# Optimization experiments

Hardware: AMD Instinct MI355X
Metric: run time of the kernel (lower is better)

Reference implementation:

```python
import jax, jax.numpy as jnp
import numpy as np

N = 50000      # nodes
E = 600000     # edges (avg degree 12)
D_IN = 16      # node_input_size
D = 128        # hidden_size
H = 4          # num_heads
DH = D // H
L = 4          # message_passing_num
D_FF = 512     # 4*hidden FFN expansion
D_OUT = 3      # output_size


def setup_inputs() -> dict:
    key = jax.random.key(0)
    ks = iter(jax.random.split(key, 32))
    def w(shape, fan_in):
        return jax.random.normal(next(ks), shape, jnp.float32) / np.float32(np.sqrt(fan_in))
    return {
        "features": jax.random.normal(next(ks), (N, D_IN), jnp.float32),
        "senders": jax.random.randint(next(ks), (E,), 0, N),
        "receivers": jax.random.randint(next(ks), (E,), 0, N),
        "enc_w1": w((D_IN, D), D_IN), "enc_b1": jnp.zeros((D,), jnp.float32),
        "enc_w2": w((D, D), D),       "enc_b2": jnp.zeros((D,), jnp.float32),
        "wq": w((L, D, D), D), "wk": w((L, D, D), D),
        "wv": w((L, D, D), D), "wo": w((L, D, D), D),
        "ln1_s": jnp.ones((L, D), jnp.float32), "ln1_b": jnp.zeros((L, D), jnp.float32),
        "ffn_w1": w((L, D, D_FF), D), "ffn_b1": jnp.zeros((L, D_FF), jnp.float32),
        "ffn_w2": w((L, D_FF, D), D_FF), "ffn_b2": jnp.zeros((L, D), jnp.float32),
        "ln2_s": jnp.ones((L, D), jnp.float32), "ln2_b": jnp.zeros((L, D), jnp.float32),
        "dec_w1": w((D, D_OUT), D), "dec_b1": jnp.zeros((D_OUT,), jnp.float32),
        "dec_w2": w((D_OUT, D_OUT), D_OUT), "dec_b2": jnp.zeros((D_OUT,), jnp.float32),
    }


def _ln(x, s, b):
    mu = x.mean(-1, keepdims=True)
    var = ((x - mu) ** 2).mean(-1, keepdims=True)
    return (x - mu) * jax.lax.rsqrt(var + 1e-5) * s + b


def _graph_mha(x, senders, receivers, wq, wk, wv, wo):
    # Adjacency-masked attention done sparsely over the edge list
    # (equivalent to softmax over the BCOO adjacency pattern).
    n = x.shape[0]
    q = (x @ wq).reshape(n, H, DH)
    k = (x @ wk).reshape(n, H, DH)
    v = (x @ wv).reshape(n, H, DH)
    scores = (q[receivers] * k[senders]).sum(-1) / np.float32(np.sqrt(DH))  # [E,H]
    m = jax.ops.segment_max(scores, receivers, num_segments=n)             # [N,H]
    m = jnp.where(jnp.isfinite(m), m, 0.0)
    a = jnp.exp(scores - m[receivers])                                      # [E,H]
    denom = jax.ops.segment_sum(a, receivers, num_segments=n)              # [N,H]
    msg = jax.ops.segment_sum(a[:, :, None] * v[senders], receivers, num_segments=n)  # [N,H,DH]
    out = (msg / (denom[:, :, None] + 1e-9)).reshape(n, D)
    return out @ wo


def reference(features, senders, receivers,
              enc_w1, enc_b1, enc_w2, enc_b2,
              wq, wk, wv, wo, ln1_s, ln1_b,
              ffn_w1, ffn_b1, ffn_w2, ffn_b2, ln2_s, ln2_b,
              dec_w1, dec_b1, dec_w2, dec_b2):
    # encode
    x = jnp.maximum(features @ enc_w1 + enc_b1, 0.0) @ enc_w2 + enc_b2     # [N,D]
    # process: L pre-LN sparse-attention transformer blocks
    for l in range(L):
        h = _ln(x, ln1_s[l], ln1_b[l])
        x = x + _graph_mha(h, senders, receivers, wq[l], wk[l], wv[l], wo[l])
        h = _ln(x, ln2_s[l], ln2_b[l])
        x = x + jnp.maximum(h @ ffn_w1[l] + ffn_b1[l], 0.0) @ ffn_w2[l] + ffn_b2[l]
    # decode
    return jnp.maximum(x @ dec_w1 + dec_b1, 0.0) @ dec_w2 + dec_b2         # [N,D_OUT]
```

## Files before the change

kernel.cpp:

```cpp
#include <hip/hip_runtime.h>
#include <hip/hip_bf16.h>
#include <math.h>

#define D     128
#define NHEAD 4
#define DH    32
#define DFF   512
#define DIN   16
#define MAXDEG 64
#define TN    16

typedef __attribute__((ext_vector_type(8))) short bf16x8;
typedef __attribute__((ext_vector_type(4))) float f32x4;
typedef __hip_bfloat16 bf16;

#define QSCALE_L2E 0.2550348838f

#define AP 132
#define BM 64

__global__ void k_fill(const int* __restrict__ recv, const int* __restrict__ senders,
                       int* __restrict__ deg, int* __restrict__ eid, int E) {
    int e = blockIdx.x * blockDim.x + threadIdx.x;
    if (e >= E) return;
    int r = recv[e];
    int pos = atomicAdd(&deg[r], 1);
    if (pos < MAXDEG) eid[r * MAXDEG + pos] = senders[e];
}

__global__ void k_wt(const float* __restrict__ wq, const float* __restrict__ wk,
                     const float* __restrict__ wv, const float* __restrict__ wo,
                     const float* __restrict__ w1, const float* __restrict__ w2,
                     const float* __restrict__ encw2,
                     bf16* __restrict__ wqkvT, bf16* __restrict__ woT,
                     bf16* __restrict__ w1T, bf16* __restrict__ w2T,
                     bf16* __restrict__ encw2T, int* __restrict__ deg, int N) {
    int r = blockIdx.y;
    if (r == 25) {
        int i = blockIdx.x * blockDim.x + threadIdx.x;
        if (i < N) deg[i] = 0;
        return;
    }
    const float* src; bf16* dst; int K, Nout;
    if (r < 12) {
        int l = r / 3, sel = r % 3;
        src = (sel == 0 ? wq : sel == 1 ? wk : wv) + (size_t)l * D * D;
        dst = wqkvT + (size_t)l * 3 * D * D + (size_t)sel * D * D;
        K = D; Nout = D;
    } else if (r < 16) {
        int l = r - 12;
        src = wo + (size_t)l * D * D; dst = woT + (size_t)l * D * D; K = D; Nout = D;
    } else if (r < 20) {
        int l = r - 16;
        src = w1 + (size_t)l * D * DFF; dst = w1T + (size_t)l * D * DFF; K = D; Nout = DFF;
    } else if (r < 24) {
        int l = r - 20;
        src = w2 + (size_t)l * DFF * D; dst = w2T + (size_t)l * DFF * D; K = DFF; Nout = D;
    } else {
        src = encw2; dst = encw2T; K = D; Nout = D;
    }
    int total = K * Nout;
    int i = blockIdx.x * blockDim.x + threadIdx.x;
    if (i >= total) return;
    int k = i / Nout, j = i % Nout;
    dst[(size_t)j * K + k] = __float2bfloat16(src[i]);
}

__device__ __forceinline__ void load_afrag(const bf16* A, int arow, int quad,
                                           int N, bf16x8* afr) {
    const bf16* ab = A + (size_t)arow * D + quad * 8;
#pragma unroll
    for (int i = 0; i < 4; i++) {
        uint4 v = make_uint4(0u, 0u, 0u, 0u);
        if (arow < N) v = *(const uint4*)(ab + i * 32);
        afr[i] = *(bf16x8*)&v;
    }
}

template<int OP>
__global__ __launch_bounds__(256) void k_gemm(
        const bf16* __restrict__ A, const bf16* __restrict__ Bt,
        const float* __restrict__ bias,
        const float* __restrict__ lns, const float* __restrict__ lnb,
        float* x, bf16* outB, int N) {
    __shared__ alignas(16) bf16 Wsm[128][AP];
    int m0 = blockIdx.x * BM;
    int t = threadIdx.x;
    int wave = t >> 6, lane = t & 63;
    int quad = lane >> 4, l16 = lane & 15;
    int wm = wave * 16;

    bf16x8 afr[4];
    load_afrag(A, m0 + wm + l16, quad, N, afr);
#pragma unroll
    for (int it = 0; it < 8; it++) {
        int ci = it * 256 + t;
        int rr = ci >> 4, cc = (ci & 15) * 8;
        *(uint4*)&Wsm[rr][cc] = *(const uint4*)(Bt + (size_t)rr * D + cc);
    }
    __syncthreads();

    f32x4 acc[8];
#pragma unroll
    for (int j = 0; j < 8; j++) acc[j] = (f32x4){0.f, 0.f, 0.f, 0.f};
#pragma unroll
    for (int i = 0; i < 4; i++) {
#pragma unroll
        for (int j = 0; j < 8; j++) {
            bf16x8 bfr = *(const bf16x8*)&Wsm[j * 16 + l16][i * 32 + quad * 8];
            acc[j] = __builtin_amdgcn_mfma_f32_16x16x32_bf16(afr[i], bfr, acc[j], 0, 0, 0);
        }
    }

    int rowb = m0 + wm + quad * 4;
    float bv[8];
    if (OP == 5) {
#pragma unroll
        for (int j = 0; j < 8; j++) bv[j] = bias[j * 16 + l16];
    }
#pragma unroll
    for (int j = 0; j < 8; j++) {
        int col = j * 16 + l16;
#pragma unroll
        for (int r = 0; r < 4; r++) {
            int gr = rowb + r;
            if (gr >= N) continue;
            float val = acc[j][r];
            if (OP == 5) val += bv[j];
            if (OP == 2) val += x[(size_t)gr * D + col];
            acc[j][r] = val;
        }
    }
    float lsv[8], lbv[8];
#pragma unroll
    for (int j = 0; j < 8; j++) {
        lsv[j] = lns[j * 16 + l16];
        lbv[j] = lnb[j * 16 + l16];
    }
#pragma unroll
    for (int r = 0; r < 4; r++) {
        float s1 = 0.f, s2 = 0.f;
#pragma unroll
        for (int j = 0; j < 8; j++) {
            float v = acc[j][r];
            s1 += v; s2 += v * v;
        }
        s1 += __shfl_xor(s1, 1, 64);  s2 += __shfl_xor(s2, 1, 64);
        s1 += __shfl_xor(s1, 2, 64);  s2 += __shfl_xor(s2, 2, 64);
        s1 += __shfl_xor(s1, 4, 64);  s2 += __shfl_xor(s2, 4, 64);
        s1 += __shfl_xor(s1, 8, 64);  s2 += __shfl_xor(s2, 8, 64);
        float mu = s1 * (1.f / 128.f);
        float var = s2 * (1.f / 128.f) - mu * mu;
        float rinv = rsqrtf(fmaxf(var, 0.f) + 1e-5f);
        int gr = rowb + r;
        if (gr >= N) continue;
#pragma unroll
        for (int j = 0; j < 8; j++) {
            int col = j * 16 + l16;
            float v = acc[j][r];
            x[(size_t)gr * D + col] = v;
            outB[(size_t)gr * D + col] =
                __float2bfloat16((v - mu) * rinv * lsv[j] + lbv[j]);
        }
    }
}

__global__ __launch_bounds__(256) void k_qkv(
        const bf16* __restrict__ hb, const bf16* __restrict__ wqkvT,
        bf16* __restrict__ qb, bf16* __restrict__ kvb, int N) {
    __shared__ alignas(16) bf16 Wsm[128][AP];
    int m0 = blockIdx.x * BM;
    int t = threadIdx.x;
    int wave = t >> 6, lane = t & 63;
    int quad = lane >> 4, l16 = lane & 15;
    int wm = wave * 16;

    bf16x8 afr[4];
    load_afrag(hb, m0 + wm + l16, quad, N, afr);

    for (int y = 0; y < 3; y++) {
        const bf16* W = wqkvT + (size_t)y * D * D;
#pragma unroll
        for (int it = 0; it < 8; it++) {
            int ci = it * 256 + t;
            int rr = ci >> 4, cc = (ci & 15) * 8;
            *(uint4*)&Wsm[rr][cc] = *(const uint4*)(W + (size_t)rr * D + cc);
        }
        __syncthreads();

        f32x4 acc[8];
#pragma unroll
        for (int j = 0; j < 8; j++) acc[j] = (f32x4){0.f, 0.f, 0.f, 0.f};
#pragma unroll
        for (int i = 0; i < 4; i++) {
#pragma unroll
            for (int j = 0; j < 8; j++) {
                bf16x8 bfr = *(const bf16x8*)&Wsm[j * 16 + l16][i * 32 + quad * 8];
                acc[j] = __builtin_amdgcn_mfma_f32_16x16x32_bf16(afr[i], bfr, acc[j], 0, 0, 0);
            }
        }
        int rowb = m0 + wm + quad * 4;
#pragma unroll
        for (int j = 0; j < 8; j++) {
            int col = j * 16 + l16;
#pragma unroll
            for (int r = 0; r < 4; r++) {
                int gr = rowb + r;
                if (gr >= N) continue;
                float val = acc[j][r];
                if (y == 0) qb[(size_t)gr * D + col] = __float2bfloat16(val * QSCALE_L2E);
                else kvb[((size_t)gr * D + col) * 2 + (y - 1)] = __float2bfloat16(val);
            }
        }
        if (y < 2) __syncthreads();
    }
}

template<int MODE>
__global__ __launch_bounds__(256) void k_ffn(
        const bf16* __restrict__ hb, const bf16* __restrict__ w1T,
        const float* __restrict__ b1,
        const bf16* __restrict__ w2T, const float* __restrict__ b2,
        const float* __restrict__ lns, const float* __restrict__ lnb,
        const float* __restrict__ dw1, const float* __restrict__ db1,
        const float* __restrict__ dw2, const float* __restrict__ db2,
        float* x, bf16* outB, float* out, int N) {
    __shared__ alignas(16) bf16 Wsm[128][AP];
    __shared__ alignas(16) bf16 Hsm[64][AP];
    int m0 = blockIdx.x * 64;
    int t = threadIdx.x;
    int wave = t >> 6, lane = t & 63;
    int quad = lane >> 4, l16 = lane & 15;
    int wm = wave * 16;

    bf16x8 afr[4];
    load_afrag(hb, m0 + wm + l16, quad, N, afr);
#pragma unroll
    for (int it = 0; it < 8; it++) {
        int ci = it * 256 + t;
        int rr = ci >> 4, cc = (ci & 15) * 8;
        *(uint4*)&Wsm[rr][cc] = *(const uint4*)(w1T + (size_t)rr * D + cc);
    }
    __syncthreads();

    f32x4 acc2[8];
#pragma unroll
    for (int j = 0; j < 8; j++) acc2[j] = (f32x4){0.f, 0.f, 0.f, 0.f};

    for (int c = 0; c < 4; c++) {
        f32x4 accP[8];
#pragma unroll
        for (int j = 0; j < 8; j++) accP[j] = (f32x4){0.f, 0.f, 0.f, 0.f};
#pragma unroll
        for (int i = 0; i < 4; i++) {
#pragma unroll
            for (int j = 0; j < 8; j++) {
                bf16x8 bfr = *(const bf16x8*)&Wsm[j * 16 + l16][i * 32 + quad * 8];
                accP[j] = __builtin_amdgcn_mfma_f32_16x16x32_bf16(afr[i], bfr, accP[j], 0, 0, 0);
            }
        }
        __syncthreads();
#pragma unroll
        for (int it = 0; it < 8; it++) {
            int ci = it * 256 + t;
            int rr = ci >> 4, cc = (ci & 15) * 8;
            *(uint4*)&Wsm[rr][cc] = *(const uint4*)(w2T + (size_t)rr * DFF + c * 128 + cc);
        }
        {
            float bv[8];
#pragma unroll
            for (int j = 0; j < 8; j++) bv[j] = b1[c * 128 + j * 16 + l16];
            int rw = wm + quad * 4;
#pragma unroll
            for (int j = 0; j < 8; j++) {
                int col = j * 16 + l16;
#pragma unroll
                for (int r = 0; r < 4; r++)
                    Hsm[rw + r][col] = __float2bfloat16(fmaxf(accP[j][r] + bv[j], 0.f));
            }
        }
        __syncthreads();
#pragma unroll
        for (int ks = 0; ks < 4; ks++) {
            bf16x8 af2 = *(const bf16x8*)&Hsm[wm + l16][ks * 32 + quad * 8];
#pragma unroll
            for (int j = 0; j < 8; j++) {
                bf16x8 bfr = *(const bf16x8*)&Wsm[j * 16 + l16][ks * 32 + quad * 8];
                acc2[j] = __builtin_amdgcn_mfma_f32_16x16x32_bf16(af2, bfr, acc2[j], 0, 0, 0);
            }
        }
        if (c < 3) {
            __syncthreads();
#pragma unroll
            for (int it = 0; it < 8; it++) {
                int ci = it * 256 + t;
                int rr = ci >> 4, cc = (ci & 15) * 8;
                *(uint4*)&Wsm[rr][cc] =
                    *(const uint4*)(w1T + (size_t)((c + 1) * 128 + rr) * D + cc);
            }
            __syncthreads();
        }
    }

    int rowb = m0 + wm + quad * 4;
    float bv[8];
#pragma unroll
    for (int j = 0; j < 8; j++) bv[j] = b2[j * 16 + l16];
#pragma unroll
    for (int j = 0; j < 8; j++) {
        int col = j * 16 + l16;
#pragma unroll
        for (int r = 0; r < 4; r++) {
            int gr = rowb + r;
            if (gr >= N) continue;
            acc2[j][r] += bv[j] + x[(size_t)gr * D + col];
        }
    }
    if (MODE == 1) {
        float dw[8][3];
#pragma unroll
        for (int j = 0; j < 8; j++) {
            int col = j * 16 + l16;
#pragma unroll
            for (int cc3 = 0; cc3 < 3; cc3++) dw[j][cc3] = dw1[col * 3 + cc3];
        }
#pragma unroll
        for (int r = 0; r < 4; r++) {
            float s0 = 0.f, s1 = 0.f, s2 = 0.f;
#pragma unroll
            for (int j = 0; j < 8; j++) {
                float v = acc2[j][r];
                s0 += v * dw[j][0]; s1 += v * dw[j][1]; s2 += v * dw[j][2];
            }
            s0 += __shfl_xor(s0, 1, 64); s1 += __shfl_xor(s1, 1, 64); s2 += __shfl_xor(s2, 1, 64);
            s0 += __shfl_xor(s0, 2, 64); s1 += __shfl_xor(s1, 2, 64); s2 += __shfl_xor(s2, 2, 64);
            s0 += __shfl_xor(s0, 4, 64); s1 += __shfl_xor(s1, 4, 64); s2 += __shfl_xor(s2, 4, 64);
            s0 += __shfl_xor(s0, 8, 64); s1 += __shfl_xor(s1, 8, 64); s2 += __shfl_xor(s2, 8, 64);
            int gr = rowb + r;
            if (l16 == 0 && gr < N) {
                float t0 = fmaxf(s0 + db1[0], 0.f);
                float t1 = fmaxf(s1 + db1[1], 0.f);
                float t2 = fmaxf(s2 + db1[2], 0.f);
#pragma unroll
                for (int o = 0; o < 3; o++)
                    out[(size_t)gr * 3 + o] =
                        t0 * dw2[0 * 3 + o] + t1 * dw2[1 * 3 + o] + t2 * dw2[2 * 3 + o] + db2[o];
            }
        }
        return;
    }
    float lsv[8], lbv[8];
#pragma unroll
    for (int j = 0; j < 8; j++) {
        lsv[j] = lns[j * 16 + l16];
        lbv[j] = lnb[j * 16 + l16];
    }
#pragma unroll
    for (int r = 0; r < 4; r++) {
        float s1 = 0.f, s2 = 0.f;
#pragma unroll
        for (int j = 0; j < 8; j++) {
            float v = acc2[j][r];
            s1 += v; s2 += v * v;
        }
        s1 += __shfl_xor(s1, 1, 64);  s2 += __shfl_xor(s2, 1, 64);
        s1 += __shfl_xor(s1, 2, 64);  s2 += __shfl_xor(s2, 2, 64);
        s1 += __shfl_xor(s1, 4, 64);  s2 += __shfl_xor(s2, 4, 64);
        s1 += __shfl_xor(s1, 8, 64);  s2 += __shfl_xor(s2, 8, 64);
        float mu = s1 * (1.f / 128.f);
        float var = s2 * (1.f / 128.f) - mu * mu;
        float rinv = rsqrtf(fmaxf(var, 0.f) + 1e-5f);
        int gr = rowb + r;
        if (gr >= N) continue;
#pragma unroll
        for (int j = 0; j < 8; j++) {
            int col = j * 16 + l16;
            float v = acc2[j][r];
            x[(size_t)gr * D + col] = v;
            outB[(size_t)gr * D + col] = __float2bfloat16((v - mu) * rinv * lsv[j] + lbv[j]);
        }
    }
}

__global__ void k_enc1(const float* __restrict__ feat,
                       const float* __restrict__ w1, const float* __restrict__ b1,
                       bf16* __restrict__ hb, int N) {
    __shared__ float fsh[TN][DIN];
    int n0 = blockIdx.x * TN;
    int j = threadIdx.x;
    int nvalid = min(TN, N - n0);
    for (int idx = j; idx < TN * DIN; idx += 128) {
        int n = idx / DIN, i = idx % DIN;
        fsh[n][i] = (n < nvalid) ? feat[(n0 + n) * DIN + i] : 0.f;
    }
    __syncthreads();
    float bb = b1[j];
#pragma unroll
    for (int n = 0; n < TN; n++) {
        float a = bb;
#pragma unroll
        for (int i = 0; i < DIN; i++) a += fsh[n][i] * w1[i * D + j];
        if (n < nvalid) hb[(size_t)(n0 + n) * D + j] = __float2bfloat16(fmaxf(a, 0.f));
    }
}

__device__ __forceinline__ void attn_edge(uint4 w, bool v, float4 qv,
                                          float& l, float& a0, float& a1,
                                          float& a2, float& a3) {
    float k0 = __uint_as_float(w.x << 16), v0 = __uint_as_float(w.x & 0xFFFF0000u);
    float k1 = __uint_as_float(w.y << 16), v1 = __uint_as_float(w.y & 0xFFFF0000u);
    float k2 = __uint_as_float(w.z << 16), v2 = __uint_as_float(w.z & 0xFFFF0000u);
    float k3 = __uint_as_float(w.w << 16), v3 = __uint_as_float(w.w & 0xFFFF0000u);
    float p = qv.x * k0 + qv.y * k1 + qv.z * k2 + qv.w * k3;
    p += __shfl_xor(p, 1, 64);
    p += __shfl_xor(p, 2, 64);
    p += __shfl_xor(p, 4, 64);
    float e = v ? exp2f(p) : 0.f;
    l += e;
    a0 += e * v0; a1 += e * v1; a2 += e * v2; a3 += e * v3;
}

__global__ __launch_bounds__(256) void k_attn(
        const bf16* __restrict__ qb, const uint* __restrict__ kvb,
        const int* __restrict__ deg, const int* __restrict__ eid,
        bf16* __restrict__ out, int N) {
    int wave = threadIdx.x >> 6, lane = threadIdx.x & 63;
    int r = blockIdx.x * 4 + wave;
    if (r >= N) return;
    int g = lane & 7;
    int h = (lane >> 3) & 3;
    int slot = lane >> 5;
    int d0 = h * 32 + g * 4;
    uint2 qw = *(const uint2*)(qb + (size_t)r * D + d0);
    float4 qv;
    qv.x = __uint_as_float(qw.x << 16);
    qv.y = __uint_as_float(qw.x & 0xFFFF0000u);
    qv.z = __uint_as_float(qw.y << 16);
    qv.w = __uint_as_float(qw.y & 0xFFFF0000u);
    int cnt = min(deg[r], MAXDEG);
    const int* row = eid + (size_t)r * MAXDEG;
    float l = 0.f, a0 = 0.f, a1 = 0.f, a2 = 0.f, a3 = 0.f;
    for (int base = 0; base < cnt; base += 8) {
        int ei[4];
        bool vv[4];
        int ss[4];
#pragma unroll
        for (int u = 0; u < 4; u++) {
            ei[u] = base + u * 2 + slot;
            vv[u] = ei[u] < cnt;
            ss[u] = vv[u] ? row[ei[u]] : 0;
        }
        uint4 w0 = *(const uint4*)(kvb + (size_t)ss[0] * D + d0);
        uint4 w1 = *(const uint4*)(kvb + (size_t)ss[1] * D + d0);
        uint4 w2 = *(const uint4*)(kvb + (size_t)ss[2] * D + d0);
        uint4 w3 = *(const uint4*)(kvb + (size_t)ss[3] * D + d0);
        attn_edge(w0, vv[0], qv, l, a0, a1, a2, a3);
        attn_edge(w1, vv[1], qv, l, a0, a1, a2, a3);
        attn_edge(w2, vv[2], qv, l, a0, a1, a2, a3);
        attn_edge(w3, vv[3], qv, l, a0, a1, a2, a3);
    }
    l  += __shfl_xor(l, 32, 64);
    a0 += __shfl_xor(a0, 32, 64);
    a1 += __shfl_xor(a1, 32, 64);
    a2 += __shfl_xor(a2, 32, 64);
    a3 += __shfl_xor(a3, 32, 64);
    if (lane < 32) {
        float inv = 1.f / (l + 1e-9f);
        bf16 o[4];
        o[0] = __float2bfloat16(a0 * inv);
        o[1] = __float2bfloat16(a1 * inv);
        o[2] = __float2bfloat16(a2 * inv);
        o[3] = __float2bfloat16(a3 * inv);
        *(uint2*)(out + (size_t)r * D + d0) = *(uint2*)o;
    }
}

extern "C" void kernel_launch(void* const* d_in, const int* in_sizes, int n_in,
                              void* d_out, int out_size, void* d_ws, size_t ws_size,
                              hipStream_t stream) {
    const float* feat    = (const float*)d_in[0];
    const int*   senders = (const int*)d_in[1];
    const int*   recv    = (const int*)d_in[2];
    const float* enc_w1  = (const float*)d_in[3];
    const float* enc_b1  = (const float*)d_in[4];
    const float* enc_w2  = (const float*)d_in[5];
    const float* enc_b2  = (const float*)d_in[6];
    const float* wq      = (const float*)d_in[7];
    const float* wk      = (const float*)d_in[8];
    const float* wv      = (const float*)d_in[9];
    const float* wo      = (const float*)d_in[10];
    const float* ln1_s   = (const float*)d_in[11];
    const float* ln1_b   = (const float*)d_in[12];
    const float* ffn_w1  = (const float*)d_in[13];
    const float* ffn_b1  = (const float*)d_in[14];
    const float* ffn_w2  = (const float*)d_in[15];
    const float* ffn_b2  = (const float*)d_in[16];
    const float* ln2_s   = (const float*)d_in[17];
    const float* ln2_b   = (const float*)d_in[18];
    const float* dec_w1  = (const float*)d_in[19];
    const float* dec_b1  = (const float*)d_in[20];
    const float* dec_w2  = (const float*)d_in[21];
    const float* dec_b2  = (const float*)d_in[22];

    int N = in_sizes[0] / DIN;
    int E = in_sizes[1];

    char* p = (char*)d_ws;
    float* x   = (float*)p;  p += (size_t)N * D * 4;
    bf16*  qb  = (bf16*)p;   p += (size_t)N * D * 2;
    bf16*  kvb = (bf16*)p;   p += (size_t)N * D * 2 * 2;
    bf16*  hb  = (bf16*)p;   p += (size_t)N * D * 2;
    int* deg   = (int*)p;    p += (size_t)N * 4;
    int* eid   = (int*)p;    p += (size_t)N * MAXDEG * 4;
    bf16* wqkvT  = (bf16*)p; p += (size_t)4 * 3 * D * D * 2;
    bf16* woT    = (bf16*)p; p += (size_t)4 * D * D * 2;
    bf16* w1T    = (bf16*)p; p += (size_t)4 * D * DFF * 2;
    bf16* w2T    = (bf16*)p; p += (size_t)4 * DFF * D * 2;
    bf16* encw2T = (bf16*)p; p += (size_t)D * D * 2;

    int gm = (N + BM - 1) / BM;

    k_wt<<<dim3(256, 26), 256, 0, stream>>>(wq, wk, wv, wo, ffn_w1, ffn_w2, enc_w2,
                                            wqkvT, woT, w1T, w2T, encw2T, deg, N);
    k_fill<<<(E + 255) / 256, 256, 0, stream>>>(recv, senders, deg, eid, E);
    k_enc1<<<(N + TN - 1) / TN, 128, 0, stream>>>(feat, enc_w1, enc_b1, hb, N);
    k_gemm<5><<<gm, 256, 0, stream>>>(hb, encw2T, enc_b2, ln1_s, ln1_b, x, hb, N);

    for (int l = 0; l < 4; l++) {
        k_qkv<<<gm, 256, 0, stream>>>(hb, wqkvT + (size_t)l * 3 * D * D, qb, kvb, N);
        k_attn<<<(N + 3) / 4, 256, 0, stream>>>(qb, (const uint*)kvb, deg, eid, hb, N);
        k_gemm<2><<<gm, 256, 0, stream>>>(hb, woT + (size_t)l * D * D,
                                          nullptr, ln2_s + l * D, ln2_b + l * D,
                                          x, hb, N);
        if (l < 3)
            k_ffn<0><<<gm, 256, 0, stream>>>(hb, w1T + (size_t)l * D * DFF,
                                             ffn_b1 + l * DFF,
                                             w2T + (size_t)l * DFF * D, ffn_b2 + l * D,
                                             ln1_s + (l + 1) * D, ln1_b + (l + 1) * D,
                                             nullptr, nullptr, nullptr, nullptr,
                                             x, hb, nullptr, N);
        else
            k_ffn<1><<<gm, 256, 0, stream>>>(hb, w1T + (size_t)l * D * DFF,
                                             ffn_b1 + l * DFF,
                                             w2T + (size_t)l * DFF * D, ffn_b2 + l * D,
                                             nullptr, nullptr,
                                             dec_w1, dec_b1, dec_w2, dec_b2,
                                             x, nullptr, (float*)d_out, N);
    }
}
```

Measured before the change: 728.5 us.

## Stage GEMM weights via async global-to-LDS loads with swizzle and multi-buffering

Replaces register-staged weight copies into padded LDS with direct global_load_lds transfers into XOR-swizzled unpadded tiles. The QKV kernel double-buffers the three weight matrices and the FFN kernel runs a 16-step, triple-buffered half-tile pipeline so weight loads overlap MFMA work. It also prefetches residual x values early, packs K/V stores into one 32-bit write, and raises wave priority around MFMA sections. The intent is to hide weight-load latency and cut LDS bank conflicts. In exchange it relies on hand-placed vmcnt waits and barriers, which are fragile if the load counts change.

```diff
diff --git a/kernel.cpp b/kernel.cpp
--- a/kernel.cpp
+++ b/kernel.cpp
@@ -16,8 +16,23 @@
 
 #define QSCALE_L2E 0.2550348838f
 
-#define AP 132
 #define BM 64
+
+#define WAITV(N) asm volatile("s_waitcnt vmcnt(" #N ")" ::: "memory")
+#define WAITLGKM asm volatile("s_waitcnt lgkmcnt(0)" ::: "memory")
+#define FENCE()  asm volatile("" ::: "memory")
+#define BAR() do { FENCE(); __builtin_amdgcn_s_barrier(); FENCE(); } while (0)
+
+__device__ __forceinline__ void gll16(const bf16* g, bf16* l) {
+    __builtin_amdgcn_global_load_lds((__attribute__((address_space(1))) void*)g,
+                                     (__attribute__((address_space(3))) void*)l,
+                                     16, 0, 0);
+}
+
+__device__ __forceinline__ ushort bfbits(float f) {
+    __hip_bfloat16 b = __float2bfloat16(f);
+    return *(ushort*)&b;
+}
 
 __global__ void k_fill(const int* __restrict__ recv, const int* __restrict__ senders,
                        int* __restrict__ deg, int* __restrict__ eid, int E) {
@@ -77,13 +92,48 @@
     }
 }
 
+__device__ __forceinline__ void stage_full(bf16* lb, const bf16* src,
+                                           int wave, int lane) {
+#pragma unroll
+    for (int k = 0; k < 8; k++) {
+        int gidx = (wave * 8 + k) * 64 + lane;
+        int r = gidx >> 4, gL = gidx & 15;
+        gll16(src + (size_t)r * 128 + ((gL ^ (r & 15)) * 8),
+              lb + (size_t)(wave * 8 + k) * 512);
+    }
+}
+
+__device__ __forceinline__ void stage_half(bf16* lb, const bf16* src, int rs,
+                                           int wave, int lane) {
+#pragma unroll
+    for (int k = 0; k < 4; k++) {
+        int gidx = (wave * 4 + k) * 64 + lane;
+        int r = gidx >> 3, gL = gidx & 7;
+        gll16(src + (size_t)r * rs + ((gL ^ (r & 7)) * 8),
+              lb + (size_t)(wave * 4 + k) * 512);
+    }
+}
+
+__device__ __forceinline__ void mfma_tile(const bf16* Wb, const bf16x8* afr,
+                                          f32x4* acc, int l16, int quad) {
+#pragma unroll
+    for (int i = 0; i < 4; i++)
+#pragma unroll
+        for (int j = 0; j < 8; j++) {
+            const bf16* wp = Wb + (size_t)(j * 16 + l16) * 128
+                              + (size_t)((((i * 4 + quad)) ^ l16) * 8);
+            acc[j] = __builtin_amdgcn_mfma_f32_16x16x32_bf16(afr[i], *(const bf16x8*)wp,
+                                                             acc[j], 0, 0, 0);
+        }
+}
+
 template<int OP>
 __global__ __launch_bounds__(256) void k_gemm(
         const bf16* __restrict__ A, const bf16* __restrict__ Bt,
         const float* __restrict__ bias,
         const float* __restrict__ lns, const float* __restrict__ lnb,
         float* x, bf16* outB, int N) {
-    __shared__ alignas(16) bf16 Wsm[128][AP];
+    __shared__ alignas(16) bf16 Wsm[128 * 128];
     int m0 = blockIdx.x * BM;
     int t = threadIdx.x;
     int wave = t >> 6, lane = t & 63;
@@ -92,27 +142,27 @@
 
     bf16x8 afr[4];
     load_afrag(A, m0 + wm + l16, quad, N, afr);
-#pragma unroll
-    for (int it = 0; it < 8; it++) {
-        int ci = it * 256 + t;
-        int rr = ci >> 4, cc = (ci & 15) * 8;
-        *(uint4*)&Wsm[rr][cc] = *(const uint4*)(Bt + (size_t)rr * D + cc);
-    }
-    __syncthreads();
+    FENCE();
+    stage_full(Wsm, Bt, wave, lane);
+    WAITV(0); BAR();
+
+    int rowb = m0 + wm + quad * 4;
+    float xv[8][4];
+    if (OP == 2) {
+#pragma unroll
+        for (int j = 0; j < 8; j++)
+#pragma unroll
+            for (int r = 0; r < 4; r++) {
+                int gr = rowb + r;
+                xv[j][r] = (gr < N) ? x[(size_t)gr * D + j * 16 + l16] : 0.f;
+            }
+    }
 
     f32x4 acc[8];
 #pragma unroll
     for (int j = 0; j < 8; j++) acc[j] = (f32x4){0.f, 0.f, 0.f, 0.f};
-#pragma unroll
-    for (int i = 0; i < 4; i++) {
-#pragma unroll
-        for (int j = 0; j < 8; j++) {
-            bf16x8 bfr = *(const bf16x8*)&Wsm[j * 16 + l16][i * 32 + quad * 8];
-            acc[j] = __builtin_amdgcn_mfma_f32_16x16x32_bf16(afr[i], bfr, acc[j], 0, 0, 0);
-        }
-    }
-
-    int rowb = m0 + wm + quad * 4;
+    mfma_tile(Wsm, afr, acc, l16, quad);
+
     float bv[8];
     if (OP == 5) {
 #pragma unroll
@@ -120,14 +170,13 @@
     }
 #pragma unroll
     for (int j = 0; j < 8; j++) {
-        int col = j * 16 + l16;
 #pragma unroll
         for (int r = 0; r < 4; r++) {
             int gr = rowb + r;
             if (gr >= N) continue;
             float val = acc[j][r];
             if (OP == 5) val += bv[j];
-            if (OP == 2) val += x[(size_t)gr * D + col];
+            if (OP == 2) val += xv[j][r];
             acc[j][r] = val;
         }
     }
@@ -168,7 +217,7 @@
 __global__ __launch_bounds__(256) void k_qkv(
         const bf16* __restrict__ hb, const bf16* __restrict__ wqkvT,
         bf16* __restrict__ qb, bf16* __restrict__ kvb, int N) {
-    __shared__ alignas(16) bf16 Wsm[128][AP];
+    __shared__ alignas(16) bf16 Wbuf[2][128 * 128];
     int m0 = blockIdx.x * BM;
     int t = threadIdx.x;
     int wave = t >> 6, lane = t & 63;
@@ -177,43 +226,59 @@
 
     bf16x8 afr[4];
     load_afrag(hb, m0 + wm + l16, quad, N, afr);
-
-    for (int y = 0; y < 3; y++) {
-        const bf16* W = wqkvT + (size_t)y * D * D;
-#pragma unroll
-        for (int it = 0; it < 8; it++) {
-            int ci = it * 256 + t;
-            int rr = ci >> 4, cc = (ci & 15) * 8;
-            *(uint4*)&Wsm[rr][cc] = *(const uint4*)(W + (size_t)rr * D + cc);
-        }
-        __syncthreads();
-
-        f32x4 acc[8];
-#pragma unroll
-        for (int j = 0; j < 8; j++) acc[j] = (f32x4){0.f, 0.f, 0.f, 0.f};
-#pragma unroll
-        for (int i = 0; i < 4; i++) {
-#pragma unroll
-            for (int j = 0; j < 8; j++) {
-                bf16x8 bfr = *(const bf16x8*)&Wsm[j * 16 + l16][i * 32 + quad * 8];
-                acc[j] = __builtin_amdgcn_mfma_f32_16x16x32_bf16(afr[i], bfr, acc[j], 0, 0, 0);
-            }
-        }
-        int rowb = m0 + wm + quad * 4;
-#pragma unroll
-        for (int j = 0; j < 8; j++) {
-            int col = j * 16 + l16;
-#pragma unroll
-            for (int r = 0; r < 4; r++) {
-                int gr = rowb + r;
-                if (gr >= N) continue;
-                float val = acc[j][r];
-                if (y == 0) qb[(size_t)gr * D + col] = __float2bfloat16(val * QSCALE_L2E);
-                else kvb[((size_t)gr * D + col) * 2 + (y - 1)] = __float2bfloat16(val);
-            }
-        }
-        if (y < 2) __syncthreads();
-    }
+    FENCE();
+    stage_full(Wbuf[0], wqkvT, wave, lane);
+    FENCE();
+    stage_full(Wbuf[1], wqkvT + (size_t)D * D, wave, lane);
+    FENCE();
+
+    f32x4 aq[8], ak[8], av[8];
+#pragma unroll
+    for (int j = 0; j < 8; j++) aq[j] = (f32x4){0.f, 0.f, 0.f, 0.f};
+
+    WAITV(8); BAR();
+    __builtin_amdgcn_s_setprio(1);
+    mfma_tile(Wbuf[0], afr, aq, l16, quad);
+    __builtin_amdgcn_s_setprio(0);
+    BAR();
+    stage_full(Wbuf[0], wqkvT + (size_t)2 * D * D, wave, lane);
+    FENCE();
+    WAITV(8); BAR();
+#pragma unroll
+    for (int j = 0; j < 8; j++) ak[j] = (f32x4){0.f, 0.f, 0.f, 0.f};
+    __builtin_amdgcn_s_setprio(1);
+    mfma_tile(Wbuf[1], afr, ak, l16, quad);
+    __builtin_amdgcn_s_setprio(0);
+    WAITV(0); BAR();
+#pragma unroll
+    for (int j = 0; j < 8; j++) av[j] = (f32x4){0.f, 0.f, 0.f, 0.f};
+    __builtin_amdgcn_s_setprio(1);
+    mfma_tile(Wbuf[0], afr, av, l16, quad);
+    __builtin_amdgcn_s_setprio(0);
+
+    int rowb = m0 + wm + quad * 4;
+#pragma unroll
+    for (int j = 0; j < 8; j++) {
+        int col = j * 16 + l16;
+#pragma unroll
+        for (int r = 0; r < 4; r++) {
+            int gr = rowb + r;
+            if (gr >= N) continue;
+            qb[(size_t)gr * D + col] = __float2bfloat16(aq[j][r] * QSCALE_L2E);
+            uint kv = (uint)bfbits(ak[j][r]) | ((uint)bfbits(av[j][r]) << 16);
+            *(uint*)&kvb[((size_t)gr * D + col) * 2] = kv;
+        }
+    }
+}
+
+__device__ __forceinline__ void stage_ffn_tile(int ts, const bf16* w1T,
+                                               const bf16* w2T, bf16* Wb3,
+                                               int wave, int lane) {
+    int c = ts >> 2, ph = ts & 3;
+    const bf16* src; int rs;
+    if (ph < 2) { src = w1T + (size_t)(c * 128) * 128 + ph * 64; rs = 128; }
+    else        { src = w2T + c * 128 + (ph - 2) * 64;           rs = DFF; }
+    stage_half(Wb3 + (size_t)(ts % 3) * (64 * 128), src, rs, wave, lane);
 }
 
 template<int MODE>
@@ -225,95 +290,115 @@
         const float* __restrict__ dw1, const float* __restrict__ db1,
         const float* __restrict__ dw2, const float* __restrict__ db2,
         float* x, bf16* outB, float* out, int N) {
-    __shared__ alignas(16) bf16 Wsm[128][AP];
-    __shared__ alignas(16) bf16 Hsm[64][AP];
+    __shared__ alignas(16) bf16 Wb3[3][64 * 128];
+    __shared__ alignas(16) bf16 Hsm[64 * 128];
     int m0 = blockIdx.x * 64;
     int t = threadIdx.x;
     int wave = t >> 6, lane = t & 63;
     int quad = lane >> 4, l16 = lane & 15;
     int wm = wave * 16;
+    int rowb = m0 + wm + quad * 4;
+
+    float b1pre[4][8];
+#pragma unroll
+    for (int c2 = 0; c2 < 4; c2++)
+#pragma unroll
+        for (int j = 0; j < 8; j++) b1pre[c2][j] = b1[c2 * 128 + j * 16 + l16];
 
     bf16x8 afr[4];
     load_afrag(hb, m0 + wm + l16, quad, N, afr);
-#pragma unroll
-    for (int it = 0; it < 8; it++) {
-        int ci = it * 256 + t;
-        int rr = ci >> 4, cc = (ci & 15) * 8;
-        *(uint4*)&Wsm[rr][cc] = *(const uint4*)(w1T + (size_t)rr * D + cc);
-    }
-    __syncthreads();
-
-    f32x4 acc2[8];
+    FENCE();
+    stage_ffn_tile(0, w1T, w2T, &Wb3[0][0], wave, lane);
+    FENCE();
+    stage_ffn_tile(1, w1T, w2T, &Wb3[0][0], wave, lane);
+    FENCE();
+
+    f32x4 acc2[8], accP[8];
 #pragma unroll
     for (int j = 0; j < 8; j++) acc2[j] = (f32x4){0.f, 0.f, 0.f, 0.f};
-
-    for (int c = 0; c < 4; c++) {
-        f32x4 accP[8];
-#pragma unroll
-        for (int j = 0; j < 8; j++) accP[j] = (f32x4){0.f, 0.f, 0.f, 0.f};
-#pragma unroll
-        for (int i = 0; i < 4; i++) {
-#pragma unroll
-            for (int j = 0; j < 8; j++) {
-                bf16x8 bfr = *(const bf16x8*)&Wsm[j * 16 + l16][i * 32 + quad * 8];
-                accP[j] = __builtin_amdgcn_mfma_f32_16x16x32_bf16(afr[i], bfr, accP[j], 0, 0, 0);
+    float xv[8][4];
+
+#pragma unroll
+    for (int s = 0; s < 16; s++) {
+        if (s < 15) { WAITV(4); } else { WAITV(0); }
+        BAR();
+        if (s + 2 < 16) {
+            stage_ffn_tile(s + 2, w1T, w2T, &Wb3[0][0], wave, lane);
+            FENCE();
+        }
+        const bf16* Wb = &Wb3[0][0] + (size_t)(s % 3) * (64 * 128);
+        int c = s >> 2, ph = s & 3;
+        if (s == 15) {
+#pragma unroll
+            for (int j = 0; j < 8; j++)
+#pragma unroll
+                for (int r = 0; r < 4; r++) {
+                    int gr = rowb + r;
+                    xv[j][r] = (gr < N) ? x[(size_t)gr * D + j * 16 + l16] : 0.f;
+                }
+        }
+        if (ph < 2) {
+            if (ph == 0) {
+#pragma unroll
+                for (int j = 0; j < 8; j++) accP[j] = (f32x4){0.f, 0.f, 0.f, 0.f};
             }
-        }
-        __syncthreads();
-#pragma unroll
-        for (int it = 0; it < 8; it++) {
-            int ci = it * 256 + t;
-            int rr = ci >> 4, cc = (ci & 15) * 8;
-            *(uint4*)&Wsm[rr][cc] = *(const uint4*)(w2T + (size_t)rr * DFF + c * 128 + cc);
-        }
-        {
-            float bv[8];
-#pragma unroll
-            for (int j = 0; j < 8; j++) bv[j] = b1[c * 128 + j * 16 + l16];
-            int rw = wm + quad * 4;
-#pragma unroll
-            for (int j = 0; j < 8; j++) {
-                int col = j * 16 + l16;
-#pragma unroll
-                for (int r = 0; r < 4; r++)
-                    Hsm[rw + r][col] = __float2bfloat16(fmaxf(accP[j][r] + bv[j], 0.f));
+            __builtin_amdgcn_s_setprio(1);
+#pragma unroll
+            for (int i2 = 0; i2 < 2; i2++) {
+#pragma unroll
+                for (int j = 0; j < 8; j++) {
+                    const bf16* wp = Wb + (size_t)(j * 16 + l16) * 64
+                                      + (size_t)(((i2 * 4 + quad) ^ (l16 & 7)) * 8);
+                    accP[j] = __builtin_amdgcn_mfma_f32_16x16x32_bf16(
+                        afr[ph * 2 + i2], *(const bf16x8*)wp, accP[j], 0, 0, 0);
+                }
             }
-        }
-        __syncthreads();
-#pragma unroll
-        for (int ks = 0; ks < 4; ks++) {
-            bf16x8 af2 = *(const bf16x8*)&Hsm[wm + l16][ks * 32 + quad * 8];
-#pragma unroll
-            for (int j = 0; j < 8; j++) {
-                bf16x8 bfr = *(const bf16x8*)&Wsm[j * 16 + l16][ks * 32 + quad * 8];
-                acc2[j] = __builtin_amdgcn_mfma_f32_16x16x32_bf16(af2, bfr, acc2[j], 0, 0, 0);
+            __builtin_amdgcn_s_setprio(0);
+            if (ph == 1) {
+                int rw = wm + quad * 4;
+#pragma unroll
+                for (int j = 0; j < 8; j++) {
+                    int gb = j * 2 + (l16 >> 3), ce = l16 & 7;
+#pragma unroll
+                    for (int r = 0; r < 4; r++) {
+                        int row = rw + r;
+                        Hsm[(size_t)row * 128 + (size_t)((gb ^ (row & 15)) * 8) + ce] =
+                            __float2bfloat16(fmaxf(accP[j][r] + b1pre[c][j], 0.f));
+                    }
+                }
+                WAITLGKM;
             }
-        }
-        if (c < 3) {
-            __syncthreads();
-#pragma unroll
-            for (int it = 0; it < 8; it++) {
-                int ci = it * 256 + t;
-                int rr = ci >> 4, cc = (ci & 15) * 8;
-                *(uint4*)&Wsm[rr][cc] =
-                    *(const uint4*)(w1T + (size_t)((c + 1) * 128 + rr) * D + cc);
+        } else {
+            int h = ph - 2;
+            __builtin_amdgcn_s_setprio(1);
+#pragma unroll
+            for (int k2 = 0; k2 < 2; k2++) {
+                int ks = h * 2 + k2;
+                const bf16* hp = Hsm + (size_t)(wm + l16) * 128
+                                  + (size_t)(((ks * 4 + quad) ^ l16) * 8);
+                bf16x8 af2 = *(const bf16x8*)hp;
+#pragma unroll
+                for (int j = 0; j < 8; j++) {
+                    const bf16* wp = Wb + (size_t)(j * 16 + l16) * 64
+                                      + (size_t)(((k2 * 4 + quad) ^ (l16 & 7)) * 8);
+                    acc2[j] = __builtin_amdgcn_mfma_f32_16x16x32_bf16(
+                        af2, *(const bf16x8*)wp, acc2[j], 0, 0, 0);
+                }
             }
-            __syncthreads();
-        }
-    }
-
-    int rowb = m0 + wm + quad * 4;
+            __builtin_amdgcn_s_setprio(0);
+        }
+    }
+
     float bv[8];
 #pragma unroll
     for (int j = 0; j < 8; j++) bv[j] = b2[j * 16 + l16];
 #pragma unroll
     for (int j = 0; j < 8; j++) {
-        int col = j * 16 + l16;
 #pragma unroll
         for (int r = 0; r < 4; r++) {
             int gr = rowb + r;
             if (gr >= N) continue;
-            acc2[j][r] += bv[j] + x[(size_t)gr * D + col];
+            acc2[j][r] += bv[j] + xv[j][r];
         }
     }
     if (MODE == 1) {
```

Result: faster. 641.2 us (-12.0%).
